# Performance work log

Hardware: AMD Instinct MI355X
Metric: run time of the kernel (lower is better)

The kernel has to match this reference:

```python
import jax, jax.numpy as jnp
import numpy as np

NH, NP, HD = 8, 4, 32  # num_heads, num_points, head_dim (C=256)


def setup_inputs() -> dict:
    key = jax.random.key(0)
    k = jax.random.split(key, 8)
    B, Nq, H, W, C = 4, 8192, 128, 128, 256
    query = jax.random.normal(k[0], (B, Nq, C), jnp.float32)
    reference_points = jax.random.uniform(k[1], (B, Nq, 2), jnp.float32)
    value = jax.random.normal(k[2], (B, H * W, C), jnp.float32)
    s = 1.0 / np.sqrt(C).astype(np.float32)
    W_off = jax.random.normal(k[3], (C, NH * NP * 2), jnp.float32) * s
    b_off = jax.random.normal(k[4], (NH * NP * 2,), jnp.float32) * 0.5
    W_attn = jax.random.normal(k[5], (C, NH * NP), jnp.float32) * s
    b_attn = jnp.zeros((NH * NP,), jnp.float32)
    W_val = jax.random.normal(k[6], (C, C), jnp.float32) * s
    b_val = jnp.zeros((C,), jnp.float32)
    W_out = jax.random.normal(k[7], (C, C), jnp.float32) * s
    b_out = jnp.zeros((C,), jnp.float32)
    return dict(query=query, reference_points=reference_points, value=value,
                W_off=W_off, b_off=b_off, W_attn=W_attn, b_attn=b_attn,
                W_val=W_val, b_val=b_val, W_out=W_out, b_out=b_out, Hs=H, Ws=W)


def reference(query, reference_points, value, W_off, b_off, W_attn, b_attn,
              W_val, b_val, W_out, b_out, Hs, Ws):
    B, Nq, C = query.shape
    # sampling offsets and attention weights from queries
    off = (query @ W_off + b_off).reshape(B, Nq, NH, NP, 2)
    attn = jax.nn.softmax((query @ W_attn + b_attn).reshape(B, Nq, NH, NP), axis=-1)
    off = jnp.stack([off[..., 0] / Ws * 0.1, off[..., 1] / Hs * 0.1], axis=-1)
    loc = jnp.clip(reference_points[:, :, None, None, :] + off, 0.0, 1.0)  # [B,Nq,NH,NP,2] (x,y)
    # project value and arrange per head: [B, NH, H*W, HD]
    v = (value @ W_val + b_val).reshape(B, Hs, Ws, NH, HD)
    v = v.transpose(0, 3, 1, 2, 4).reshape(B, NH, Hs * Ws, HD)
    # grid_sample bilinear, align_corners=False, padding_mode='border':
    # pixel coord = loc*size - 0.5, clamped to [0, size-1]
    gx = jnp.clip(loc[..., 0] * Ws - 0.5, 0.0, Ws - 1.0)
    gy = jnp.clip(loc[..., 1] * Hs - 0.5, 0.0, Hs - 1.0)
    x0 = jnp.floor(gx); y0 = jnp.floor(gy)
    fx = gx - x0; fy = gy - y0
    x0i = x0.astype(jnp.int32); y0i = y0.astype(jnp.int32)
    x1i = jnp.minimum(x0i + 1, Ws - 1); y1i = jnp.minimum(y0i + 1, Hs - 1)

    def flat(xi, yi):  # [B,Nq,NH,NP] -> [B,NH,Nq*NP]
        return (yi * Ws + xi).transpose(0, 2, 1, 3).reshape(B, NH, Nq * NP)

    def gather(idx):  # -> [B,NH,Nq*NP,HD]
        return jnp.take_along_axis(v, idx[..., None], axis=2)

    def wts(w):  # [B,Nq,NH,NP] -> [B,NH,Nq*NP,1]
        return w.transpose(0, 2, 1, 3).reshape(B, NH, Nq * NP, 1)

    samp = (wts((1 - fx) * (1 - fy)) * gather(flat(x0i, y0i))
            + wts(fx * (1 - fy)) * gather(flat(x1i, y0i))
            + wts((1 - fx) * fy) * gather(flat(x0i, y1i))
            + wts(fx * fy) * gather(flat(x1i, y1i)))
    samp = samp.reshape(B, NH, Nq, NP, HD)
    aw = attn.transpose(0, 2, 1, 3)[..., None]  # [B,NH,Nq,NP,1]
    out = (samp * aw).sum(axis=3)               # [B,NH,Nq,HD]
    out = out.transpose(0, 2, 1, 3).reshape(B, Nq, C)
    return out @ W_out + b_out
```

## Files before the change

kernel.cpp:

```cpp
#include <hip/hip_runtime.h>
#include <cstddef>

#define B_   4
#define NQ_  8192
#define C_   256
#define H_   128
#define W_   128
#define HW_  (H_ * W_)
#define NH_  8
#define NP_  4
#define HD_  32

typedef __attribute__((ext_vector_type(8))) short s16x8;
typedef __attribute__((ext_vector_type(4))) float f32x4;

__device__ __forceinline__ short f2bf(float x) {
    unsigned u = __float_as_uint(x);
    unsigned r = (u + 0x7FFFu + ((u >> 16) & 1u)) >> 16;
    return (short)r;
}
__device__ __forceinline__ unsigned cvt_pk_bf16(float lo, float hi) {
    unsigned r;
    asm("v_cvt_pk_bf16_f32 %0, %1, %2" : "=v"(r) : "v"(lo), "v"(hi));
    return r;
}
__device__ __forceinline__ void gload_lds16(const void* g, void* l) {
    __builtin_amdgcn_global_load_lds(
        (const __attribute__((address_space(1))) void*)g,
        (__attribute__((address_space(3))) void*)l, 16, 0, 0);
}

__global__ void prep_kernel(const float* __restrict__ Wv, const float* __restrict__ Wo,
                            const float* __restrict__ Woff, const float* __restrict__ Wattn,
                            const float* __restrict__ boff, const float* __restrict__ battn,
                            short* __restrict__ BtVal, short* __restrict__ BtOut,
                            short* __restrict__ BtOA, float* __restrict__ biasOA)
{
    const int b = blockIdx.x, t = threadIdx.x;
    if (b < 256) {
        const int n = b;
        BtVal[(size_t)n * 256 + t] = f2bf(Wv[(size_t)t * 256 + n]);
    } else if (b < 512) {
        const int n = b - 256;
        BtOut[(size_t)n * 256 + t] = f2bf(Wo[(size_t)t * 256 + n]);
    } else {
        const int n = b - 512;
        float v = (n < 64) ? Woff[(size_t)t * 64 + n]
                           : (n < 96 ? Wattn[(size_t)t * 32 + (n - 64)] : 0.f);
        BtOA[(size_t)n * 256 + t] = f2bf(v);
        if (t == 0) biasOA[n] = (n < 64) ? boff[n] : (n < 96 ? battn[n - 64] : 0.f);
    }
}

template<int ADT>
__device__ __forceinline__ void gemm_body(
    const void* __restrict__ Ap, const short* __restrict__ Bt,
    const float* __restrict__ bias, void* __restrict__ Cp,
    int ldc, int omode, int m0, int n0, char* AsRaw, short* Bs)
{
    constexpr int ABYTES = (ADT == 1) ? 16384 : 8192;
    const int tid = threadIdx.x;
    const int l = tid & 63;
    const int w = tid >> 6;
    const int wm = w >> 1, wn = w & 1;

    f32x4 acc[4][4];
#pragma unroll
    for (int i = 0; i < 4; ++i)
#pragma unroll
        for (int j = 0; j < 4; ++j) acc[i][j] = (f32x4)0.f;

    const int frag_r = l & 15;
    const int kslot  = (l >> 4) * 8;
    const float* Af  = (const float*)Ap;
    const short* A16 = (const short*)Ap;

#define STAGE_B(k0, buf)                                                      \
    _Pragma("unroll")                                                         \
    for (int r = 0; r < 2; ++r) {                                             \
        const int i = r * 256 + tid;                                          \
        gload_lds16(&Bt[(size_t)(n0 + (i >> 2)) * 256 + (k0) + (i & 3) * 8],  \
                    (char*)Bs + (buf) * 8192 + r * 4096 + w * 1024);          \
    }
#define STAGE_A(k0, buf)                                                      \
    if (ADT == 0) {                                                           \
        _Pragma("unroll")                                                     \
        for (int r = 0; r < 2; ++r) {                                         \
            const int i = r * 256 + tid;                                      \
            gload_lds16(&A16[(size_t)(m0 + (i >> 2)) * 256 + (k0) + (i & 3) * 8], \
                        AsRaw + (buf) * ABYTES + r * 4096 + w * 1024);        \
        }                                                                     \
    } else {                                                                  \
        _Pragma("unroll")                                                     \
        for (int r = 0; r < 4; ++r) {                                         \
            const int i = r * 256 + tid;                                      \
            const int row = i >> 3, s = i & 7;                                \
            const int colf = (s * 4) ^ ((row & 7) << 2);      \
            gload_lds16(&Af[(size_t)(m0 + row) * 256 + (k0) + colf],          \
                        AsRaw + (buf) * ABYTES + r * 4096 + w * 1024);        \
        }                                                                     \
    }

    STAGE_B(0, 0);
    STAGE_A(0, 0);
    __syncthreads();

#pragma unroll
    for (int k = 0; k < 8; ++k) {
        const int cur = k & 1, nxt = cur ^ 1;
        if (k < 7) {
            STAGE_B((k + 1) * 32, nxt);
            STAGE_A((k + 1) * 32, nxt);
        }
        s16x8 a[4], b[4];
#pragma unroll
        for (int mf = 0; mf < 4; ++mf) {
            const int row = wm * 64 + mf * 16 + frag_r;
            if (ADT == 0) {
                a[mf] = *(const s16x8*)(AsRaw + cur * ABYTES + row * 64 + kslot * 2);
            } else {
                const int g0 = (l >> 4) * 2;
                const char* base = AsRaw + cur * ABYTES + row * 128;
                const float4 q0 = *(const float4*)(base + ((g0 * 16)       ^ ((row & 7) << 4)));
                const float4 q1 = *(const float4*)(base + (((g0 + 1) * 16) ^ ((row & 7) << 4)));
                union { unsigned u[4]; s16x8 v; } pk;
                pk.u[0] = cvt_pk_bf16(q0.x, q0.y);
                pk.u[1] = cvt_pk_bf16(q0.z, q0.w);
                pk.u[2] = cvt_pk_bf16(q1.x, q1.y);
                pk.u[3] = cvt_pk_bf16(q1.z, q1.w);
                a[mf] = pk.v;
            }
        }
#pragma unroll
        for (int nf = 0; nf < 4; ++nf)
            b[nf] = *(const s16x8*)&Bs[cur * 4096 + (wn * 64 + nf * 16 + frag_r) * 32 + kslot];
#pragma unroll
        for (int mf = 0; mf < 4; ++mf)
#pragma unroll
            for (int nf = 0; nf < 4; ++nf)
                acc[mf][nf] = __builtin_amdgcn_mfma_f32_16x16x32_bf16(
                    a[mf], b[nf], acc[mf][nf], 0, 0, 0);
        if (k < 7) __syncthreads();
    }
#undef STAGE_B
#undef STAGE_A

    const int col_local = wn * 64 + (l & 15);
    const int rbase = wm * 64 + (l >> 4) * 4;
    if (omode == 0) {
#pragma unroll
        for (int nf = 0; nf < 4; ++nf) {
            const int n = n0 + col_local + nf * 16;
            const float bs = bias[n];
#pragma unroll
            for (int mf = 0; mf < 4; ++mf) {
                const f32x4 v = acc[mf][nf];
#pragma unroll
                for (int rr = 0; rr < 4; ++rr)
                    ((float*)Cp)[(size_t)(m0 + rbase + mf * 16 + rr) * ldc + n] = v[rr] + bs;
            }
        }
    } else {
#pragma unroll
        for (int nf = 0; nf < 4; ++nf) {
            const int n = n0 + col_local + nf * 16;
            const float bs = bias[n];
            const int h = n >> 5, d = n & 31;
#pragma unroll
            for (int mf = 0; mf < 4; ++mf) {
                const f32x4 v = acc[mf][nf];
#pragma unroll
                for (int rr = 0; rr < 4; ++rr) {
                    const int m = m0 + rbase + mf * 16 + rr;
                    const int bb = m >> 14, pix = m & (HW_ - 1);
                    ((short*)Cp)[((size_t)(bb * NH_ + h) * HW_ + pix) * HD_ + d] = f2bf(v[rr] + bs);
                }
            }
        }
    }
}

__global__ __launch_bounds__(256, 3)
void gemm_k1k2a(const float* __restrict__ value, const short* __restrict__ BtVal,
                const float* __restrict__ b_val, short* __restrict__ vproj,
                const float* __restrict__ query, const short* __restrict__ BtOA,
                const float* __restrict__ biasOA, float* __restrict__ oa)
{
    __shared__ char  AsRaw[2 * 16384];
    __shared__ short Bs[2 * 4096];
    const int bid = blockIdx.x;
    if (bid < 1024) {
        gemm_body<1>(value, BtVal, b_val, vproj, 0, 2,
                     (bid >> 1) * 128, (bid & 1) * 128, AsRaw, Bs);
    } else {
        gemm_body<1>(query, BtOA, biasOA, oa, 128, 0,
                     (bid - 1024) * 128, 0, AsRaw, Bs);
    }
}

__global__ __launch_bounds__(256, 4)
void gemm_k3(const short* __restrict__ samp, const short* __restrict__ BtOut,
             const float* __restrict__ b_out, float* __restrict__ out)
{
    __shared__ char  AsRaw[2 * 8192];
    __shared__ short Bs[2 * 4096];
    gemm_body<0>(samp, BtOut, b_out, out, 256, 0,
                 (blockIdx.x >> 1) * 128, (blockIdx.x & 1) * 128, AsRaw, Bs);
}

__global__ __launch_bounds__(256)
void sample_kernel(const float* __restrict__ oa,
                   const float* __restrict__ ref,
                   const short* __restrict__ vproj,
                   short* __restrict__ samp)
{
    __shared__ int4   s_idx[2][32];
    __shared__ float4 s_w[2][32];
    const int tid = threadIdx.x;
    const int q0 = blockIdx.x * 2;

    if (tid < 64) {
        const int qq = tid >> 5;
        const int hp = tid & 31;
        const int h = hp >> 2, p = hp & 3;
        const int q = q0 + qq;
        const float logit = oa[(size_t)q * 128 + 64 + h * 4 + p];
        float mx = fmaxf(logit, __shfl_xor(logit, 1));
        mx = fmaxf(mx, __shfl_xor(mx, 2));
        float e = __expf(logit - mx);
        float s = e + __shfl_xor(e, 1);
        s += __shfl_xor(s, 2);
        const float aw = e / s;

        const float ox = oa[(size_t)q * 128 + h * 8 + p * 2 + 0] * (0.1f / (float)W_);
        const float oy = oa[(size_t)q * 128 + h * 8 + p * 2 + 1] * (0.1f / (float)H_);
        const float lx = fminf(fmaxf(ref[(size_t)q * 2 + 0] + ox, 0.f), 1.f);
        const float ly = fminf(fmaxf(ref[(size_t)q * 2 + 1] + oy, 0.f), 1.f);
        const float gx = fminf(fmaxf(lx * (float)W_ - 0.5f, 0.f), (float)(W_ - 1));
        const float gy = fminf(fmaxf(ly * (float)H_ - 0.5f, 0.f), (float)(H_ - 1));
        const float x0f = floorf(gx), y0f = floorf(gy);
        const float fx = gx - x0f, fy = gy - y0f;
        const int x0 = (int)x0f, y0 = (int)y0f;
        const int x1 = min(x0 + 1, W_ - 1), y1 = min(y0 + 1, H_ - 1);
        s_idx[qq][hp] = make_int4((y0 * W_ + x0) * HD_, (y0 * W_ + x1) * HD_,
                                  (y1 * W_ + x0) * HD_, (y1 * W_ + x1) * HD_);
        const float gx1 = 1.f - fx, gy1 = 1.f - fy;
        s_w[qq][hp] = make_float4(aw * gx1 * gy1, aw * fx * gy1,
                                  aw * gx1 * fy,  aw * fx * fy);
    }
    __syncthreads();

    const int qq = tid >> 7;
    const int t = tid & 127;
    const int h = t >> 4;
    const int d0 = (t & 15) * 2;
    const int q = q0 + qq;
    const int b = q >> 13;
    const short* vh = vproj + (size_t)(b * NH_ + h) * (HW_ * HD_) + d0;

    float a0 = 0.f, a1 = 0.f;
#pragma unroll
    for (int p = 0; p < 4; ++p) {
        const int4   ii = s_idx[qq][h * 4 + p];
        const float4 ww = s_w[qq][h * 4 + p];
        unsigned v;
        v = *(const unsigned*)&vh[ii.x];
        a0 = fmaf(ww.x, __uint_as_float(v << 16), a0);
        a1 = fmaf(ww.x, __uint_as_float(v & 0xFFFF0000u), a1);
        v = *(const unsigned*)&vh[ii.y];
        a0 = fmaf(ww.y, __uint_as_float(v << 16), a0);
        a1 = fmaf(ww.y, __uint_as_float(v & 0xFFFF0000u), a1);
        v = *(const unsigned*)&vh[ii.z];
        a0 = fmaf(ww.z, __uint_as_float(v << 16), a0);
        a1 = fmaf(ww.z, __uint_as_float(v & 0xFFFF0000u), a1);
        v = *(const unsigned*)&vh[ii.w];
        a0 = fmaf(ww.w, __uint_as_float(v << 16), a0);
        a1 = fmaf(ww.w, __uint_as_float(v & 0xFFFF0000u), a1);
    }
    const unsigned lo = (unsigned)(unsigned short)f2bf(a0);
    const unsigned hi = (unsigned)(unsigned short)f2bf(a1);
    ((unsigned*)samp)[((size_t)q * 256 + h * HD_ + d0) >> 1] = lo | (hi << 16);
}

extern "C" void kernel_launch(void* const* d_in, const int* in_sizes, int n_in,
                              void* d_out, int out_size, void* d_ws, size_t ws_size,
                              hipStream_t stream)
{
    const float* query  = (const float*)d_in[0];
    const float* refpt  = (const float*)d_in[1];
    const float* value  = (const float*)d_in[2];
    const float* W_off  = (const float*)d_in[3];
    const float* b_off  = (const float*)d_in[4];
    const float* W_attn = (const float*)d_in[5];
    const float* b_attn = (const float*)d_in[6];
    const float* W_val  = (const float*)d_in[7];
    const float* b_val  = (const float*)d_in[8];
    const float* W_out  = (const float*)d_in[9];
    const float* b_out  = (const float*)d_in[10];
    float* out = (float*)d_out;

    char* ws = (char*)d_ws;
    short* vproj  = (short*)ws;
    short* samp   = (short*)(ws + (size_t)32 * 1024 * 1024);
    float* oa     = (float*)(ws + (size_t)48 * 1024 * 1024);
    short* BtVal  = (short*)(ws + (size_t)64 * 1024 * 1024);
    short* BtOut  = BtVal + 256 * 256;
    short* BtOA   = BtOut + 256 * 256;
    float* biasOA = (float*)(BtOA + 128 * 256);

    prep_kernel<<<640, 256, 0, stream>>>(W_val, W_out, W_off, W_attn,
                                         b_off, b_attn, BtVal, BtOut, BtOA, biasOA);

    gemm_k1k2a<<<1280, 256, 0, stream>>>(value, BtVal, b_val, vproj,
                                         query, BtOA, biasOA, oa);

    sample_kernel<<<(B_ * NQ_) / 2, 256, 0, stream>>>(oa, refpt, vproj, samp);

    gemm_k3<<<512, 256, 0, stream>>>(samp, BtOut, b_out, out);
}
```

Measured before the change: 79.84 us.

## Widen value/query projection GEMM tiles to full 256-column N per block

The fused value-projection and offset/attention GEMM kernel now uses 512-thread blocks covering a 128x256 output tile, so each fp32 A tile is loaded and converted to bf16 only once instead of twice across two N-halves. The query projection is padded to 256 columns (BtOA grown, prep grid enlarged) and stores skip columns beyond 96. The shared GEMM template is split into two specialized kernels. This cuts duplicate global reads of the large fp32 value/query matrices, but wastes MFMA work on the padded query columns and doubles per-block LDS for B.

```diff
diff --git a/kernel.cpp b/kernel.cpp
--- a/kernel.cpp
+++ b/kernel.cpp
@@ -52,17 +52,130 @@
     }
 }
 
-template<int ADT>
-__device__ __forceinline__ void gemm_body(
-    const void* __restrict__ Ap, const short* __restrict__ Bt,
-    const float* __restrict__ bias, void* __restrict__ Cp,
-    int ldc, int omode, int m0, int n0, char* AsRaw, short* Bs)
-{
-    constexpr int ABYTES = (ADT == 1) ? 16384 : 8192;
+__global__ __launch_bounds__(512, 4)
+void gemm_k1k2a(const float* __restrict__ value, const short* __restrict__ BtVal,
+                const float* __restrict__ b_val, short* __restrict__ vproj,
+                const float* __restrict__ query, const short* __restrict__ BtOA,
+                const float* __restrict__ biasOA, float* __restrict__ oa)
+{
+    __shared__ char  AsRaw[2 * 16384];
+    __shared__ short Bs[2 * 8192];
+    const int tid = threadIdx.x;
+    const int l = tid & 63;
+    const int w = tid >> 6;
+    const int wm = w >> 2, wn = w & 3;
+    const int bid = blockIdx.x;
+
+    const float* Af;  const short* Bt;  const float* bias;
+    int omode, m0;
+    if (bid < 512) { Af = value; Bt = BtVal; bias = b_val;  omode = 2; m0 = bid * 128; }
+    else           { Af = query; Bt = BtOA;  bias = biasOA; omode = 0; m0 = (bid - 512) * 128; }
+
+    f32x4 acc[4][4];
+#pragma unroll
+    for (int i = 0; i < 4; ++i)
+#pragma unroll
+        for (int j = 0; j < 4; ++j) acc[i][j] = (f32x4)0.f;
+
+    const int frag_r = l & 15;
+    const int kslot  = (l >> 4) * 8;
+
+#define STAGE_A(k0, buf)                                                      \
+    _Pragma("unroll")                                                         \
+    for (int r = 0; r < 2; ++r) {                                             \
+        const int i = r * 512 + tid;                                          \
+        const int row = i >> 3, s = i & 7;                                    \
+        const int colf = (s * 4) ^ ((row & 7) << 2);          \
+        gload_lds16(&Af[(size_t)(m0 + row) * 256 + (k0) + colf],              \
+                    AsRaw + (buf) * 16384 + r * 8192 + w * 1024);             \
+    }
+#define STAGE_B(k0, buf)                                                      \
+    _Pragma("unroll")                                                         \
+    for (int r = 0; r < 2; ++r) {                                             \
+        const int i = r * 512 + tid;                                          \
+        const int row = i >> 2, cb = (i & 3) * 8;                             \
+        gload_lds16(&Bt[(size_t)row * 256 + (k0) + cb],                       \
+                    (char*)Bs + (buf) * 16384 + r * 8192 + w * 1024);         \
+    }
+
+    STAGE_B(0, 0);
+    STAGE_A(0, 0);
+    __syncthreads();
+
+#pragma unroll
+    for (int k = 0; k < 8; ++k) {
+        const int cur = k & 1, nxt = cur ^ 1;
+        if (k < 7) {
+            STAGE_B((k + 1) * 32, nxt);
+            STAGE_A((k + 1) * 32, nxt);
+        }
+        s16x8 a[4], b[4];
+#pragma unroll
+        for (int mf = 0; mf < 4; ++mf) {
+            const int row = wm * 64 + mf * 16 + frag_r;
+            const int g0 = (l >> 4) * 2;
+            const char* base = AsRaw + cur * 16384 + row * 128;
+            const float4 q0 = *(const float4*)(base + ((g0 * 16)       ^ ((row & 7) << 4)));
+            const float4 q1 = *(const float4*)(base + (((g0 + 1) * 16) ^ ((row & 7) << 4)));
+            union { unsigned u[4]; s16x8 v; } pk;
+            pk.u[0] = cvt_pk_bf16(q0.x, q0.y);
+            pk.u[1] = cvt_pk_bf16(q0.z, q0.w);
+            pk.u[2] = cvt_pk_bf16(q1.x, q1.y);
+            pk.u[3] = cvt_pk_bf16(q1.z, q1.w);
+            a[mf] = pk.v;
+        }
+#pragma unroll
+        for (int nf = 0; nf < 4; ++nf)
+            b[nf] = *(const s16x8*)&Bs[cur * 8192 + (wn * 64 + nf * 16 + frag_r) * 32 + kslot];
+#pragma unroll
+        for (int mf = 0; mf < 4; ++mf)
+#pragma unroll
+            for (int nf = 0; nf < 4; ++nf)
+                acc[mf][nf] = __builtin_amdgcn_mfma_f32_16x16x32_bf16(
+                    a[mf], b[nf], acc[mf][nf], 0, 0, 0);
+        if (k < 7) __syncthreads();
+    }
+#undef STAGE_A
+#undef STAGE_B
+
+    const int col_local = wn * 64 + (l & 15);
+    const int rbase = wm * 64 + (l >> 4) * 4;
+#pragma unroll
+    for (int nf = 0; nf < 4; ++nf) {
+        const int n = col_local + nf * 16;
+        if (omode == 0 && n >= 96) continue;
+        const float bs = bias[n];
+#pragma unroll
+        for (int mf = 0; mf < 4; ++mf) {
+            const f32x4 v = acc[mf][nf];
+#pragma unroll
+            for (int rr = 0; rr < 4; ++rr) {
+                const int m = m0 + rbase + mf * 16 + rr;
+                const float o = v[rr] + bs;
+                if (omode == 0) {
+                    oa[(size_t)m * 128 + n] = o;
+                } else {
+                    const int bb = m >> 14, pix = m & (HW_ - 1);
+                    const int h = n >> 5, d = n & 31;
+                    vproj[((size_t)(bb * NH_ + h) * HW_ + pix) * HD_ + d] = f2bf(o);
+                }
+            }
+        }
+    }
+}
+
+__global__ __launch_bounds__(256, 4)
+void gemm_k3(const short* __restrict__ A16, const short* __restrict__ Bt,
+             const float* __restrict__ bias, float* __restrict__ Cp)
+{
+    __shared__ char  AsRaw[2 * 8192];
+    __shared__ short Bs[2 * 4096];
     const int tid = threadIdx.x;
     const int l = tid & 63;
     const int w = tid >> 6;
     const int wm = w >> 1, wn = w & 1;
+    const int m0 = (blockIdx.x >> 1) * 128;
+    const int n0 = (blockIdx.x & 1) * 128;
 
     f32x4 acc[4][4];
 #pragma unroll
@@ -72,65 +185,37 @@
 
     const int frag_r = l & 15;
     const int kslot  = (l >> 4) * 8;
-    const float* Af  = (const float*)Ap;
-    const short* A16 = (const short*)Ap;
-
-#define STAGE_B(k0, buf)                                                      \
+
+#define STAGE_B3(k0, buf)                                                     \
     _Pragma("unroll")                                                         \
     for (int r = 0; r < 2; ++r) {                                             \
         const int i = r * 256 + tid;                                          \
         gload_lds16(&Bt[(size_t)(n0 + (i >> 2)) * 256 + (k0) + (i & 3) * 8],  \
                     (char*)Bs + (buf) * 8192 + r * 4096 + w * 1024);          \
     }
-#define STAGE_A(k0, buf)                                                      \
-    if (ADT == 0) {                                                           \
-        _Pragma("unroll")                                                     \
-        for (int r = 0; r < 2; ++r) {                                         \
-            const int i = r * 256 + tid;                                      \
-            gload_lds16(&A16[(size_t)(m0 + (i >> 2)) * 256 + (k0) + (i & 3) * 8], \
-                        AsRaw + (buf) * ABYTES + r * 4096 + w * 1024);        \
-        }                                                                     \
-    } else {                                                                  \
-        _Pragma("unroll")                                                     \
-        for (int r = 0; r < 4; ++r) {                                         \
-            const int i = r * 256 + tid;                                      \
-            const int row = i >> 3, s = i & 7;                                \
-            const int colf = (s * 4) ^ ((row & 7) << 2);      \
-            gload_lds16(&Af[(size_t)(m0 + row) * 256 + (k0) + colf],          \
-                        AsRaw + (buf) * ABYTES + r * 4096 + w * 1024);        \
-        }                                                                     \
-    }
-
-    STAGE_B(0, 0);
-    STAGE_A(0, 0);
+#define STAGE_A3(k0, buf)                                                     \
+    _Pragma("unroll")                                                         \
+    for (int r = 0; r < 2; ++r) {                                             \
+        const int i = r * 256 + tid;                                          \
+        gload_lds16(&A16[(size_t)(m0 + (i >> 2)) * 256 + (k0) + (i & 3) * 8], \
+                    AsRaw + (buf) * 8192 + r * 4096 + w * 1024);              \
+    }
+
+    STAGE_B3(0, 0);
+    STAGE_A3(0, 0);
     __syncthreads();
 
 #pragma unroll
     for (int k = 0; k < 8; ++k) {
         const int cur = k & 1, nxt = cur ^ 1;
         if (k < 7) {
-            STAGE_B((k + 1) * 32, nxt);
-            STAGE_A((k + 1) * 32, nxt);
+            STAGE_B3((k + 1) * 32, nxt);
+            STAGE_A3((k + 1) * 32, nxt);
         }
         s16x8 a[4], b[4];
 #pragma unroll
-        for (int mf = 0; mf < 4; ++mf) {
-            const int row = wm * 64 + mf * 16 + frag_r;
-            if (ADT == 0) {
-                a[mf] = *(const s16x8*)(AsRaw + cur * ABYTES + row * 64 + kslot * 2);
-            } else {
-                const int g0 = (l >> 4) * 2;
-                const char* base = AsRaw + cur * ABYTES + row * 128;
-                const float4 q0 = *(const float4*)(base + ((g0 * 16)       ^ ((row & 7) << 4)));
-                const float4 q1 = *(const float4*)(base + (((g0 + 1) * 16) ^ ((row & 7) << 4)));
-                union { unsigned u[4]; s16x8 v; } pk;
-                pk.u[0] = cvt_pk_bf16(q0.x, q0.y);
-                pk.u[1] = cvt_pk_bf16(q0.z, q0.w);
-                pk.u[2] = cvt_pk_bf16(q1.x, q1.y);
-                pk.u[3] = cvt_pk_bf16(q1.z, q1.w);
-                a[mf] = pk.v;
-            }
-        }
+        for (int mf = 0; mf < 4; ++mf)
+            a[mf] = *(const s16x8*)(AsRaw + cur * 8192 + (wm * 64 + mf * 16 + frag_r) * 64 + kslot * 2);
 #pragma unroll
         for (int nf = 0; nf < 4; ++nf)
             b[nf] = *(const s16x8*)&Bs[cur * 4096 + (wn * 64 + nf * 16 + frag_r) * 32 + kslot];
@@ -142,70 +227,23 @@
                     a[mf], b[nf], acc[mf][nf], 0, 0, 0);
         if (k < 7) __syncthreads();
     }
-#undef STAGE_B
-#undef STAGE_A
+#undef STAGE_A3
+#undef STAGE_B3
 
     const int col_local = wn * 64 + (l & 15);
     const int rbase = wm * 64 + (l >> 4) * 4;
-    if (omode == 0) {
-#pragma unroll
-        for (int nf = 0; nf < 4; ++nf) {
-            const int n = n0 + col_local + nf * 16;
-            const float bs = bias[n];
-#pragma unroll
-            for (int mf = 0; mf < 4; ++mf) {
-                const f32x4 v = acc[mf][nf];
-#pragma unroll
-                for (int rr = 0; rr < 4; ++rr)
-                    ((float*)Cp)[(size_t)(m0 + rbase + mf * 16 + rr) * ldc + n] = v[rr] + bs;
-            }
-        }
-    } else {
-#pragma unroll
-        for (int nf = 0; nf < 4; ++nf) {
-            const int n = n0 + col_local + nf * 16;
-            const float bs = bias[n];
-            const int h = n >> 5, d = n & 31;
-#pragma unroll
-            for (int mf = 0; mf < 4; ++mf) {
-                const f32x4 v = acc[mf][nf];
-#pragma unroll
-                for (int rr = 0; rr < 4; ++rr) {
-                    const int m = m0 + rbase + mf * 16 + rr;
-                    const int bb = m >> 14, pix = m & (HW_ - 1);
-                    ((short*)Cp)[((size_t)(bb * NH_ + h) * HW_ + pix) * HD_ + d] = f2bf(v[rr] + bs);
-                }
-            }
-        }
-    }
-}
-
-__global__ __launch_bounds__(256, 3)
-void gemm_k1k2a(const float* __restrict__ value, const short* __restrict__ BtVal,
-                const float* __restrict__ b_val, short* __restrict__ vproj,
-                const float* __restrict__ query, const short* __restrict__ BtOA,
-                const float* __restrict__ biasOA, float* __restrict__ oa)
-{
-    __shared__ char  AsRaw[2 * 16384];
-    __shared__ short Bs[2 * 4096];
-    const int bid = blockIdx.x;
-    if (bid < 1024) {
-        gemm_body<1>(value, BtVal, b_val, vproj, 0, 2,
-                     (bid >> 1) * 128, (bid & 1) * 128, AsRaw, Bs);
-    } else {
-        gemm_body<1>(query, BtOA, biasOA, oa, 128, 0,
-                     (bid - 1024) * 128, 0, AsRaw, Bs);
-    }
-}
-
-__global__ __launch_bounds__(256, 4)
-void gemm_k3(const short* __restrict__ samp, const short* __restrict__ BtOut,
-             const float* __restrict__ b_out, float* __restrict__ out)
-{
-    __shared__ char  AsRaw[2 * 8192];
-    __shared__ short Bs[2 * 4096];
-    gemm_body<0>(samp, BtOut, b_out, out, 256, 0,
-                 (blockIdx.x >> 1) * 128, (blockIdx.x & 1) * 128, AsRaw, Bs);
+#pragma unroll
+    for (int nf = 0; nf < 4; ++nf) {
+        const int n = n0 + col_local + nf * 16;
+        const float bs = bias[n];
+#pragma unroll
+        for (int mf = 0; mf < 4; ++mf) {
+            const f32x4 v = acc[mf][nf];
+#pragma unroll
+            for (int rr = 0; rr < 4; ++rr)
+                Cp[(size_t)(m0 + rbase + mf * 16 + rr) * 256 + n] = v[rr] + bs;
+        }
+    }
 }
 
 __global__ __launch_bounds__(256)
@@ -306,13 +344,13 @@
     short* BtVal  = (short*)(ws + (size_t)64 * 1024 * 1024);
     short* BtOut  = BtVal + 256 * 256;
     short* BtOA   = BtOut + 256 * 256;
-    float* biasOA = (float*)(BtOA + 128 * 256);
-
-    prep_kernel<<<640, 256, 0, stream>>>(W_val, W_out, W_off, W_attn,
+    float* biasOA = (float*)(BtOA + 256 * 256);
+
+    prep_kernel<<<768, 256, 0, stream>>>(W_val, W_out, W_off, W_attn,
                                          b_off, b_attn, BtVal, BtOut, BtOA, biasOA);
 
-    gemm_k1k2a<<<1280, 256, 0, stream>>>(value, BtVal, b_val, vproj,
-                                         query, BtOA, biasOA, oa);
+    gemm_k1k2a<<<768, 512, 0, stream>>>(value, BtVal, b_val, vproj,
+                                        query, BtOA, biasOA, oa);
 
     sample_kernel<<<(B_ * NQ_) / 2, 256, 0, stream>>>(oa, refpt, vproj, samp);
 
```

Result: no change. 78.76 us (-1.4%).
